# Kernel optimization log

Measured on AMD Instinct MI355X. Metric: run time of the kernel, lower is better.

The kernel has to match this reference:

```python
import jax, jax.numpy as jnp
import numpy as np

B, S, D = 1, 2048, 2048
H, KV, HD = 32, 8, 64
POWER = 100000.0


def _rotary(x):
    # x: [B, h, S, HD]; faithful to RotaryEncoder: freqs = pos / div_term
    rot_dim = HD // 2
    pos = jnp.arange(S, dtype=x.dtype)
    div = POWER ** (jnp.arange(0, HD, 2, dtype=x.dtype) / HD)  # [HD//2]
    freqs = pos[:, None] / div  # [S, HD//2]
    cos, sin = jnp.cos(freqs), jnp.sin(freqs)
    x_rot, x_pass = x[..., :rot_dim], x[..., rot_dim:]
    h = rot_dim // 2
    rot_half = jnp.concatenate([-x_rot[..., h:], x_rot[..., :h]], axis=-1)
    return jnp.concatenate([x_rot * cos + rot_half * sin, x_pass], axis=-1)


def setup_inputs() -> dict:
    key = jax.random.key(0)
    k1, k2, k3 = jax.random.split(key, 3)
    hidden_states = jax.random.normal(k1, (B, S, D), dtype=jnp.float32)
    op_size = H * HD + 2 * KV * HD
    Wqkv = jax.random.normal(k2, (D, op_size), dtype=jnp.float32) * 0.02
    Wo = jax.random.normal(k3, (H * HD, D), dtype=jnp.float32) * 0.02
    causal = jnp.tril(jnp.ones((S, S), dtype=bool))
    attention_mask = jnp.where(causal, 0.0, -1e9).astype(jnp.float32)[None, None]
    return {"hidden_states": hidden_states, "attention_mask": attention_mask,
            "Wqkv": Wqkv, "Wo": Wo}


def reference(hidden_states, attention_mask, Wqkv, Wo):
    groups = H // KV
    qkv = hidden_states @ Wqkv  # [B, S, op_size]
    qpos = H * HD
    q = qkv[..., :qpos].reshape(B, S, H, HD).transpose(0, 2, 1, 3)
    k = qkv[..., qpos:qpos + KV * HD].reshape(B, S, KV, HD).transpose(0, 2, 1, 3)
    v = qkv[..., qpos + KV * HD:].reshape(B, S, KV, HD).transpose(0, 2, 1, 3)
    q = _rotary(q)
    k = _rotary(k)
    k = jnp.repeat(k, groups, axis=1)  # GQA repeat_interleave -> [B, H, S, HD]
    v = jnp.repeat(v, groups, axis=1)
    scores = jnp.einsum('bhqd,bhkd->bhqk', q, k) / jnp.sqrt(jnp.float32(HD))
    scores = scores + attention_mask[..., :S]
    attn = jax.nn.softmax(scores.astype(jnp.float32), axis=-1).astype(v.dtype)
    out = jnp.einsum('bhqk,bhkd->bhqd', attn, v)
    out = out.transpose(0, 2, 1, 3).reshape(B, S, H * HD)
    return out @ Wo
```

## Files before the change

kernel.cpp:

```cpp
#include <hip/hip_runtime.h>
#include <hip/hip_bf16.h>
#include <cstdint>
#include <cstddef>

#define S_LEN 2048
#define D_MODEL 2048
#define NH 32
#define NKV 8
#define HDIM 64
#define OPSZ 3072
#define KOFF 2048
#define VOFF 2560

typedef float    floatx4 __attribute__((ext_vector_type(4)));
typedef __bf16   bf16x8  __attribute__((ext_vector_type(8)));
typedef __bf16   bf16x4  __attribute__((ext_vector_type(4)));
typedef __bf16   bf16_t;
typedef _Float16 f16_t;
typedef _Float16 f16x2   __attribute__((ext_vector_type(2)));
typedef _Float16 f16x4   __attribute__((ext_vector_type(4)));
typedef _Float16 f16x8   __attribute__((ext_vector_type(8)));
typedef __fp16   hfx2    __attribute__((ext_vector_type(2)));

__device__ __forceinline__ void gld16(const void* g, void* l) {
  __builtin_amdgcn_global_load_lds((__attribute__((address_space(1))) void*)(void*)g,
                                   (__attribute__((address_space(3))) void*)l,
                                   16, 0, 0);
}

#define ACQ(N) do { asm volatile("s_waitcnt vmcnt(" #N ")" ::: "memory");        \
                    __builtin_amdgcn_s_barrier();                                \
                    __builtin_amdgcn_sched_barrier(0); } while (0)
#define REL()  do { __builtin_amdgcn_sched_barrier(0);                           \
                    __builtin_amdgcn_s_barrier();                                \
                    __builtin_amdgcn_sched_barrier(0); } while (0)

__global__ __launch_bounds__(256)
void prep_kernel(const float* __restrict__ X, const float* __restrict__ Wqkv,
                 const float* __restrict__ Wo, bf16_t* __restrict__ Xb,
                 bf16_t* __restrict__ WqkvT, bf16_t* __restrict__ WoT) {
  const int bx = blockIdx.x;
  const int k0 = blockIdx.y * 32;
  const int tx = threadIdx.x & 31, ty = threadIdx.x >> 5;
  if (bx < 160) {
    __shared__ float tile[32][33];
    const float* W; bf16_t* Wt; int N, n0;
    if (bx < 96) { W = Wqkv; Wt = WqkvT; N = OPSZ;    n0 = bx * 32; }
    else         { W = Wo;   Wt = WoT;   N = D_MODEL; n0 = (bx - 96) * 32; }
#pragma unroll
    for (int i = 0; i < 32; i += 8)
      tile[ty + i][tx] = W[(size_t)(k0 + ty + i) * N + n0 + tx];
    __syncthreads();
#pragma unroll
    for (int i = 0; i < 32; i += 8)
      Wt[(size_t)(n0 + ty + i) * D_MODEL + k0 + tx] = (bf16_t)tile[tx][ty + i];
  } else {
    const int n0 = (bx - 160) * 32;
#pragma unroll
    for (int i = 0; i < 32; i += 8) {
      const size_t idx = (size_t)(k0 + ty + i) * D_MODEL + n0 + tx;
      Xb[idx] = (bf16_t)X[idx];
    }
  }
}

#define GEMM128_CORE(A_, Bt_, K_, m0_, n0_)                                       \
  const int tid = threadIdx.x;                                                    \
  const int wave = tid >> 6;                                                      \
  const int lane = tid & 63;                                                      \
  const int lane15 = lane & 15;                                                   \
  const int quad = lane >> 4;                                                     \
  const int wm = (wave & 1) * 64;                                                 \
  const int wn = (wave >> 1) * 64;                                                \
  floatx4 acc[4][4];                                                              \
  _Pragma("unroll") for (int i = 0; i < 4; i++)                                   \
    _Pragma("unroll") for (int j = 0; j < 4; j++)                                 \
      acc[i][j] = floatx4{0.f, 0.f, 0.f, 0.f};                                    \
  {                                                                               \
    int srow[4], scol[4];                                                         \
    _Pragma("unroll") for (int i = 0; i < 4; i++) {                               \
      const int c = tid + i * 256;                                                \
      srow[i] = c >> 3;                                                           \
      scol[i] = (((c & 7) * 16) ^ ((srow[i] & 7) << 4)) >> 1;                     \
    }                                                                             \
    const bf16_t* Ab = (A_) + (size_t)(m0_) * (K_);                               \
    const bf16_t* Bb = (Bt_) + (size_t)(n0_) * (K_);                              \
    const int rsw = (lane15 & 7) << 4;                                            \
    auto stage = [&](bf16_t* dA, bf16_t* dB, int k0) {                            \
      _Pragma("unroll") for (int i = 0; i < 4; i++)                               \
        gld16(Ab + (size_t)srow[i] * (K_) + k0 + scol[i],                         \
              dA + (i * 256 + wave * 64) * 8);                                    \
      _Pragma("unroll") for (int i = 0; i < 4; i++)                               \
        gld16(Bb + (size_t)srow[i] * (K_) + k0 + scol[i],                         \
              dB + (i * 256 + wave * 64) * 8);                                    \
    };                                                                            \
    auto comp = [&](const bf16_t* sA, const bf16_t* sB) {                         \
      _Pragma("unroll") for (int kt = 0; kt < 2; kt++) {                          \
        const int off = ((kt * 64 + quad * 16) ^ rsw) >> 1;                       \
        bf16x8 af[4], bfr[4];                                                     \
        _Pragma("unroll") for (int mi = 0; mi < 4; mi++)                          \
          af[mi] = *(const bf16x8*)&sA[(wm + mi * 16 + lane15) * 64 + off];       \
        _Pragma("unroll") for (int ni = 0; ni < 4; ni++)                          \
          bfr[ni] = *(const bf16x8*)&sB[(wn + ni * 16 + lane15) * 64 + off];      \
        _Pragma("unroll") for (int mi = 0; mi < 4; mi++)                          \
          _Pragma("unroll") for (int ni = 0; ni < 4; ni++)                        \
            acc[mi][ni] = __builtin_amdgcn_mfma_f32_16x16x32_bf16(af[mi], bfr[ni],\
                                                                  acc[mi][ni], 0, 0, 0); \
      }                                                                           \
    };                                                                            \
    const int NT = (K_) / 64;                                                     \
    stage(As0, Bs0, 0);                                                           \
    stage(As1, Bs1, 64);                                                          \
    for (int t = 0; t < NT - 2; t += 2) {                                         \
      ACQ(8);                                                                     \
      comp(As0, Bs0);                                                             \
      REL();                                                                      \
      stage(As0, Bs0, (t + 2) * 64);                                              \
      ACQ(8);                                                                     \
      comp(As1, Bs1);                                                             \
      REL();                                                                      \
      stage(As1, Bs1, (t + 3) * 64);                                              \
    }                                                                             \
    ACQ(8);                                                                       \
    comp(As0, Bs0);                                                               \
    ACQ(0);                                                                       \
    comp(As1, Bs1);                                                               \
  }

#define GEMM128_LDS                                                               \
  __shared__ bf16_t As0[128 * 64];                                                \
  __shared__ bf16_t As1[128 * 64];                                                \
  __shared__ bf16_t Bs0[128 * 64];                                                \
  __shared__ bf16_t Bs1[128 * 64];

#define XCD_SWZ(m0_, n0_)                                                         \
  const int gx_ = gridDim.x;                                                      \
  const int id_ = blockIdx.y * gx_ + blockIdx.x;                                  \
  const int cpx_ = (gx_ * gridDim.y) >> 3;                                        \
  const int sid_ = (id_ & 7) * cpx_ + (id_ >> 3);                                 \
  const int m0_ = (sid_ / gx_) * 128;                                             \
  const int n0_ = (sid_ % gx_) * 128;

#define QSCALE 0.18033688011112042f
__global__ __launch_bounds__(256, 2)
void gemm_qkv_rope(const bf16_t* __restrict__ A, const bf16_t* __restrict__ Bt,
                   bf16_t* __restrict__ Qr, bf16_t* __restrict__ Kr,
                   f16_t* __restrict__ VtG) {
  GEMM128_LDS
  XCD_SWZ(m0, n0)
  GEMM128_CORE(A, Bt, D_MODEL, m0, n0)

  const int colbase = n0 + wn;
  const int s0 = m0 + wm;

  if (colbase < VOFF) {
    const bool isQ = (colbase < KOFF);
    const float k2 = 0.51905126483f;
    const float pj0 = exp2f(-(float)lane15 * k2);
    const float pj1 = pj0 * 0.0031622776601684f;
    bf16_t* dst = isQ ? (Qr + ((size_t)(colbase >> 6) * S_LEN) * HDIM)
                      : (Kr + ((size_t)((colbase - KOFF) >> 6) * S_LEN) * HDIM);
    const float qs = isQ ? QSCALE : 1.0f;
#pragma unroll
    for (int mi = 0; mi < 4; mi++) {
#pragma unroll
      for (int r = 0; r < 4; r++) {
        const int s = s0 + mi * 16 + quad * 4 + r;
        const float sf = (float)s;
        float s0s, s0c, s1s, s1c;
        __sincosf(sf * pj0, &s0s, &s0c);
        __sincosf(sf * pj1, &s1s, &s1c);
        const float x0 = acc[mi][0][r], x1 = acc[mi][1][r];
        bf16_t* row = dst + (size_t)s * HDIM + lane15;
        row[0]  = (bf16_t)((x0 * s0c - x1 * s0s) * qs);
        row[16] = (bf16_t)((x1 * s1c + x0 * s1s) * qs);
        row[32] = (bf16_t)(acc[mi][2][r] * qs);
        row[48] = (bf16_t)(acc[mi][3][r] * qs);
      }
    }
  } else {
    const int kvv = (colbase - VOFF) >> 6;
    f16_t* dst = VtG + (size_t)kvv * HDIM * S_LEN;
#pragma unroll
    for (int mi = 0; mi < 4; mi++) {
      const int s = s0 + mi * 16 + quad * 4;
#pragma unroll
      for (int ni = 0; ni < 4; ni++) {
        const int d = ni * 16 + lane15;
        f16x4 tv;
#pragma unroll
        for (int r = 0; r < 4; r++) tv[r] = (f16_t)acc[mi][ni][r];
        *(f16x4*)&dst[(size_t)d * S_LEN + s] = tv;
      }
    }
  }
}

__global__ __launch_bounds__(256, 2)
void gemm_bt_f32out(const bf16_t* __restrict__ A, const bf16_t* __restrict__ Bt,
                    float* __restrict__ C, int M, int N, int K) {
  GEMM128_LDS
  XCD_SWZ(m0, n0)
  GEMM128_CORE(A, Bt, K, m0, n0)

#pragma unroll
  for (int mi = 0; mi < 4; mi++)
#pragma unroll
    for (int r = 0; r < 4; r++) {
      const int row = m0 + wm + mi * 16 + quad * 4 + r;
#pragma unroll
      for (int ni = 0; ni < 4; ni++) {
        const int col = n0 + wn + ni * 16 + lane15;
        C[(size_t)row * N + col] = acc[mi][ni][r];
      }
    }
}

__global__ __launch_bounds__(256, 4)
void flash_kernel(const bf16_t* __restrict__ Qr, const bf16_t* __restrict__ Kr,
                  const f16_t* __restrict__ VtG, bf16_t* __restrict__ attn) {
  __shared__ bf16_t Ks[128 * 64];
  __shared__ f16_t  Vt[64 * 128];

  const int tid = threadIdx.x;
  const int wave = tid >> 6;
  const int lane = tid & 63;
  const int lane15 = lane & 15;
  const int quad = lane >> 4;
  const int bx = blockIdx.x;
  const int h = bx & 31;
  const int qblk = 31 - (bx >> 5);
  const int q0 = qblk * 64;
  const int rq = q0 + wave * 16;
  const int kv = h >> 2;
  const size_t kbase = (size_t)kv * S_LEN * HDIM;
  const size_t vbase = (size_t)kv * HDIM * S_LEN;

  const int krow0 = tid >> 3;
  const int kcol  = ((((tid & 7) * 16) ^ ((krow0 & 7) << 4)) >> 1);
  const int vd0   = tid >> 4;
  const int vcol  = ((((tid & 15) * 16) ^ ((vd0 & 15) << 4)) >> 1);

  const int kswz = (lane15 & 7) << 4;
  const int vswz = lane15 << 4;

  bf16x8 aq[2];
#pragma unroll
  for (int kt = 0; kt < 2; kt++)
    aq[kt] = *(const bf16x8*)&Qr[((size_t)h * S_LEN + rq + lane15) * HDIM + kt * 32 + quad * 8];

  const f16x4 vone = {(f16_t)1.0f, (f16_t)1.0f, (f16_t)1.0f, (f16_t)1.0f};

  floatx4 lacc = floatx4{0.f, 0.f, 0.f, 0.f};
  floatx4 o[4];
#pragma unroll
  for (int dt = 0; dt < 4; dt++) o[dt] = floatx4{0.f, 0.f, 0.f, 0.f};

  const int nk = (qblk + 2) >> 1;

  for (int t = 0; t < nk; ++t) {
    const int p0 = t * 128;
    __syncthreads();
#pragma unroll
    for (int i = 0; i < 4; i++)
      gld16(Kr + kbase + (size_t)(p0 + krow0 + i * 32) * HDIM + kcol,
            &Ks[(i * 256 + wave * 64) * 8]);
#pragma unroll
    for (int i = 0; i < 4; i++)
      gld16(VtG + vbase + (size_t)(vd0 + i * 16) * S_LEN + p0 + vcol,
            &Vt[(i * 256 + wave * 64) * 8]);
    __syncthreads();

    floatx4 sc[8];
#pragma unroll
    for (int nt = 0; nt < 8; nt++) sc[nt] = floatx4{0.f, 0.f, 0.f, 0.f};
#pragma unroll
    for (int kt = 0; kt < 2; kt++) {
#pragma unroll
      for (int nt = 0; nt < 8; nt++) {
        const bf16x8 ak = *(const bf16x8*)&Ks[(nt * 16 + lane15) * 64 +
                                              (((kt * 64 + quad * 16) ^ kswz) >> 1)];
        sc[nt] = __builtin_amdgcn_mfma_f32_16x16x32_bf16(ak, aq[kt], sc[nt], 0, 0, 0);
      }
    }

    if (p0 + 127 > rq) {
#pragma unroll
      for (int nt = 0; nt < 8; nt++)
#pragma unroll
        for (int r = 0; r < 4; r++) {
          const int kpos = p0 + nt * 16 + quad * 4 + r;
          const int qrow = rq + lane15;
          if (kpos > qrow) sc[nt][r] = -1e30f;
        }
    }

    f16x4 ph[8];
#pragma unroll
    for (int nt = 0; nt < 8; nt++) {
      const float e0 = __builtin_amdgcn_exp2f(sc[nt][0]);
      const float e1 = __builtin_amdgcn_exp2f(sc[nt][1]);
      const float e2 = __builtin_amdgcn_exp2f(sc[nt][2]);
      const float e3 = __builtin_amdgcn_exp2f(sc[nt][3]);
      const hfx2 lo_ = __builtin_amdgcn_cvt_pkrtz(e0, e1);
      const hfx2 hi_ = __builtin_amdgcn_cvt_pkrtz(e2, e3);
      const f16x2 lo = __builtin_bit_cast(f16x2, lo_);
      const f16x2 hi = __builtin_bit_cast(f16x2, hi_);
      ph[nt] = __builtin_shufflevector(lo, hi, 0, 1, 2, 3);
    }

#pragma unroll
    for (int kt4 = 0; kt4 < 8; kt4++) {
      lacc = __builtin_amdgcn_mfma_f32_16x16x16f16(vone, ph[kt4], lacc, 0, 0, 0);
#pragma unroll
      for (int dt = 0; dt < 4; dt++) {
        const f16x4 av = *(const f16x4*)&Vt[(dt * 16 + lane15) * 128 +
                                            (((kt4 * 32 + quad * 8) ^ vswz) >> 1)];
        o[dt] = __builtin_amdgcn_mfma_f32_16x16x16f16(av, ph[kt4], o[dt], 0, 0, 0);
      }
    }
  }

  const float inv = 1.0f / lacc[0];
  const int s = rq + lane15;
#pragma unroll
  for (int dt = 0; dt < 4; dt++) {
    bf16x4 tv;
#pragma unroll
    for (int r = 0; r < 4; r++) tv[r] = (bf16_t)(o[dt][r] * inv);
    *(bf16x4*)&attn[(size_t)s * D_MODEL + h * HDIM + dt * 16 + quad * 4] = tv;
  }
}

extern "C" void kernel_launch(void* const* d_in, const int* in_sizes, int n_in,
                              void* d_out, int out_size, void* d_ws, size_t ws_size,
                              hipStream_t stream) {
  (void)in_sizes; (void)n_in; (void)out_size; (void)ws_size;
  const float* hidden = (const float*)d_in[0];
  const float* Wqkv = (const float*)d_in[2];
  const float* Wo   = (const float*)d_in[3];
  float* out = (float*)d_out;

  char* ws = (char*)d_ws;
  size_t off = 0;
  auto alloc = [&](size_t bytes) -> void* {
    void* p = ws + off;
    off += (bytes + 255) & ~(size_t)255;
    return p;
  };
  bf16_t* Xb    = (bf16_t*)alloc((size_t)S_LEN * D_MODEL * 2);
  bf16_t* WqkvT = (bf16_t*)alloc((size_t)OPSZ * D_MODEL * 2);
  bf16_t* WoT   = (bf16_t*)alloc((size_t)D_MODEL * D_MODEL * 2);
  bf16_t* Qr    = (bf16_t*)alloc((size_t)NH * S_LEN * HDIM * 2);
  bf16_t* Kr    = (bf16_t*)alloc((size_t)NKV * S_LEN * HDIM * 2);
  f16_t*  VtG   = (f16_t*) alloc((size_t)NKV * HDIM * S_LEN * 2);
  bf16_t* attn  = (bf16_t*)alloc((size_t)S_LEN * D_MODEL * 2);

  prep_kernel<<<dim3(224, 64), 256, 0, stream>>>(hidden, Wqkv, Wo, Xb, WqkvT, WoT);
  gemm_qkv_rope<<<dim3(OPSZ / 128, S_LEN / 128), 256, 0, stream>>>(Xb, WqkvT, Qr, Kr, VtG);
  flash_kernel<<<dim3(32 * NH), 256, 0, stream>>>(Qr, Kr, VtG, attn);
  gemm_bt_f32out<<<dim3(D_MODEL / 128, S_LEN / 128), 256, 0, stream>>>(attn, WoT, out, S_LEN, D_MODEL, D_MODEL);
}
```

Measured before the change: 203.0 us.

## Store K and V in MFMA-fragment layout and read directly from global

The QKV GEMM epilogue now writes K and V in a pre-swizzled fragment layout that matches the MFMA operand order. The flash kernel can then load its K and V fragments straight from global memory into registers, dropping the LDS staging and both __syncthreads per tile. The cost is that each of the four waves re-reads the same K/V from global or L2 with no LDS sharing. The K/V epilogue also now uses scattered 2-byte stores.

Result: slower. 230.4 us (+13.5%).

```diff
diff --git a/kernel.cpp b/kernel.cpp
--- a/kernel.cpp
+++ b/kernel.cpp
@@ -144,8 +144,8 @@
 #define QSCALE 0.18033688011112042f
 __global__ __launch_bounds__(256, 2)
 void gemm_qkv_rope(const bf16_t* __restrict__ A, const bf16_t* __restrict__ Bt,
-                   bf16_t* __restrict__ Qr, bf16_t* __restrict__ Kr,
-                   f16_t* __restrict__ VtG) {
+                   bf16_t* __restrict__ Qr, bf16_t* __restrict__ KF,
+                   f16_t* __restrict__ VF) {
   GEMM128_LDS
   XCD_SWZ(m0, n0)
   GEMM128_CORE(A, Bt, D_MODEL, m0, n0)
@@ -153,14 +153,11 @@
   const int colbase = n0 + wn;
   const int s0 = m0 + wm;
 
-  if (colbase < VOFF) {
-    const bool isQ = (colbase < KOFF);
+  if (colbase < KOFF) {
     const float k2 = 0.51905126483f;
     const float pj0 = exp2f(-(float)lane15 * k2);
     const float pj1 = pj0 * 0.0031622776601684f;
-    bf16_t* dst = isQ ? (Qr + ((size_t)(colbase >> 6) * S_LEN) * HDIM)
-                      : (Kr + ((size_t)((colbase - KOFF) >> 6) * S_LEN) * HDIM);
-    const float qs = isQ ? QSCALE : 1.0f;
+    bf16_t* dst = Qr + ((size_t)(colbase >> 6) * S_LEN) * HDIM;
 #pragma unroll
     for (int mi = 0; mi < 4; mi++) {
 #pragma unroll
@@ -172,25 +169,51 @@
         __sincosf(sf * pj1, &s1s, &s1c);
         const float x0 = acc[mi][0][r], x1 = acc[mi][1][r];
         bf16_t* row = dst + (size_t)s * HDIM + lane15;
-        row[0]  = (bf16_t)((x0 * s0c - x1 * s0s) * qs);
-        row[16] = (bf16_t)((x1 * s1c + x0 * s1s) * qs);
-        row[32] = (bf16_t)(acc[mi][2][r] * qs);
-        row[48] = (bf16_t)(acc[mi][3][r] * qs);
+        row[0]  = (bf16_t)((x0 * s0c - x1 * s0s) * QSCALE);
+        row[16] = (bf16_t)((x1 * s1c + x0 * s1s) * QSCALE);
+        row[32] = (bf16_t)(acc[mi][2][r] * QSCALE);
+        row[48] = (bf16_t)(acc[mi][3][r] * QSCALE);
+      }
+    }
+  } else if (colbase < VOFF) {
+    const float k2 = 0.51905126483f;
+    const float pj0 = exp2f(-(float)lane15 * k2);
+    const float pj1 = pj0 * 0.0031622776601684f;
+    bf16_t* dst = KF + (size_t)((colbase - KOFF) >> 6) * (S_LEN * HDIM);
+    const int jj = lane15 & 7;
+    const int sb = lane15 >> 3;
+#pragma unroll
+    for (int mi = 0; mi < 4; mi++) {
+#pragma unroll
+      for (int r = 0; r < 4; r++) {
+        const int s = s0 + mi * 16 + quad * 4 + r;
+        const float sf = (float)s;
+        float s0s, s0c, s1s, s1c;
+        __sincosf(sf * pj0, &s0s, &s0c);
+        __sincosf(sf * pj1, &s1s, &s1c);
+        const float x0 = acc[mi][0][r], x1 = acc[mi][1][r];
+        const int t7 = s >> 7, ntq = (s >> 4) & 7;
+        const int l0 = quad * 4 + r;
+        bf16_t* pk0 = dst + ((t7 * 2 + 0) * 8 + ntq) * 512;
+        bf16_t* pk1 = dst + ((t7 * 2 + 1) * 8 + ntq) * 512;
+        pk0[(l0 + 16 * sb) * 8 + jj]       = (bf16_t)(x0 * s0c - x1 * s0s);
+        pk0[(l0 + 16 * (2 + sb)) * 8 + jj] = (bf16_t)(x1 * s1c + x0 * s1s);
+        pk1[(l0 + 16 * sb) * 8 + jj]       = (bf16_t)acc[mi][2][r];
+        pk1[(l0 + 16 * (2 + sb)) * 8 + jj] = (bf16_t)acc[mi][3][r];
       }
     }
   } else {
     const int kvv = (colbase - VOFF) >> 6;
-    f16_t* dst = VtG + (size_t)kvv * HDIM * S_LEN;
+    f16_t* dst = VF + (size_t)kvv * (S_LEN * HDIM);
 #pragma unroll
     for (int mi = 0; mi < 4; mi++) {
-      const int s = s0 + mi * 16 + quad * 4;
+      const int s16 = (s0 + mi * 16) >> 4;
 #pragma unroll
       for (int ni = 0; ni < 4; ni++) {
-        const int d = ni * 16 + lane15;
         f16x4 tv;
 #pragma unroll
         for (int r = 0; r < 4; r++) tv[r] = (f16_t)acc[mi][ni][r];
-        *(f16x4*)&dst[(size_t)d * S_LEN + s] = tv;
+        *(f16x4*)&dst[(((size_t)s16 * 4 + ni) * 64 + lane) * 4] = tv;
       }
     }
   }
@@ -217,11 +240,8 @@
 }
 
 __global__ __launch_bounds__(256, 4)
-void flash_kernel(const bf16_t* __restrict__ Qr, const bf16_t* __restrict__ Kr,
-                  const f16_t* __restrict__ VtG, bf16_t* __restrict__ attn) {
-  __shared__ bf16_t Ks[128 * 64];
-  __shared__ f16_t  Vt[64 * 128];
-
+void flash_kernel(const bf16_t* __restrict__ Qr, const bf16_t* __restrict__ KF,
+                  const f16_t* __restrict__ VF, bf16_t* __restrict__ attn) {
   const int tid = threadIdx.x;
   const int wave = tid >> 6;
   const int lane = tid & 63;
@@ -233,16 +253,9 @@
   const int q0 = qblk * 64;
   const int rq = q0 + wave * 16;
   const int kv = h >> 2;
-  const size_t kbase = (size_t)kv * S_LEN * HDIM;
-  const size_t vbase = (size_t)kv * HDIM * S_LEN;
-
-  const int krow0 = tid >> 3;
-  const int kcol  = ((((tid & 7) * 16) ^ ((krow0 & 7) << 4)) >> 1);
-  const int vd0   = tid >> 4;
-  const int vcol  = ((((tid & 15) * 16) ^ ((vd0 & 15) << 4)) >> 1);
-
-  const int kswz = (lane15 & 7) << 4;
-  const int vswz = lane15 << 4;
+
+  const bf16_t* kf = KF + (size_t)kv * (S_LEN * HDIM) + lane * 8;
+  const f16_t*  vf = VF + (size_t)kv * (S_LEN * HDIM) + lane * 4;
 
   bf16x8 aq[2];
 #pragma unroll
@@ -260,16 +273,6 @@
 
   for (int t = 0; t < nk; ++t) {
     const int p0 = t * 128;
-    __syncthreads();
-#pragma unroll
-    for (int i = 0; i < 4; i++)
-      gld16(Kr + kbase + (size_t)(p0 + krow0 + i * 32) * HDIM + kcol,
-            &Ks[(i * 256 + wave * 64) * 8]);
-#pragma unroll
-    for (int i = 0; i < 4; i++)
-      gld16(VtG + vbase + (size_t)(vd0 + i * 16) * S_LEN + p0 + vcol,
-            &Vt[(i * 256 + wave * 64) * 8]);
-    __syncthreads();
 
     floatx4 sc[8];
 #pragma unroll
@@ -278,8 +281,7 @@
     for (int kt = 0; kt < 2; kt++) {
 #pragma unroll
       for (int nt = 0; nt < 8; nt++) {
-        const bf16x8 ak = *(const bf16x8*)&Ks[(nt * 16 + lane15) * 64 +
-                                              (((kt * 64 + quad * 16) ^ kswz) >> 1)];
+        const bf16x8 ak = *(const bf16x8*)(kf + (size_t)(((t * 2 + kt) * 8 + nt)) * 512);
         sc[nt] = __builtin_amdgcn_mfma_f32_16x16x32_bf16(ak, aq[kt], sc[nt], 0, 0, 0);
       }
     }
@@ -314,8 +316,7 @@
       lacc = __builtin_amdgcn_mfma_f32_16x16x16f16(vone, ph[kt4], lacc, 0, 0, 0);
 #pragma unroll
       for (int dt = 0; dt < 4; dt++) {
-        const f16x4 av = *(const f16x4*)&Vt[(dt * 16 + lane15) * 128 +
-                                            (((kt4 * 32 + quad * 8) ^ vswz) >> 1)];
+        const f16x4 av = *(const f16x4*)(vf + (size_t)(((t * 8 + kt4) * 4 + dt)) * 256);
         o[dt] = __builtin_amdgcn_mfma_f32_16x16x16f16(av, ph[kt4], o[dt], 0, 0, 0);
       }
     }
@@ -352,12 +353,12 @@
   bf16_t* WqkvT = (bf16_t*)alloc((size_t)OPSZ * D_MODEL * 2);
   bf16_t* WoT   = (bf16_t*)alloc((size_t)D_MODEL * D_MODEL * 2);
   bf16_t* Qr    = (bf16_t*)alloc((size_t)NH * S_LEN * HDIM * 2);
-  bf16_t* Kr    = (bf16_t*)alloc((size_t)NKV * S_LEN * HDIM * 2);
-  f16_t*  VtG   = (f16_t*) alloc((size_t)NKV * HDIM * S_LEN * 2);
+  bf16_t* KF    = (bf16_t*)alloc((size_t)NKV * S_LEN * HDIM * 2);
+  f16_t*  VF    = (f16_t*) alloc((size_t)NKV * HDIM * S_LEN * 2);
   bf16_t* attn  = (bf16_t*)alloc((size_t)S_LEN * D_MODEL * 2);
 
   prep_kernel<<<dim3(224, 64), 256, 0, stream>>>(hidden, Wqkv, Wo, Xb, WqkvT, WoT);
-  gemm_qkv_rope<<<dim3(OPSZ / 128, S_LEN / 128), 256, 0, stream>>>(Xb, WqkvT, Qr, Kr, VtG);
-  flash_kernel<<<dim3(32 * NH), 256, 0, stream>>>(Qr, Kr, VtG, attn);
+  gemm_qkv_rope<<<dim3(OPSZ / 128, S_LEN / 128), 256, 0, stream>>>(Xb, WqkvT, Qr, KF, VF);
+  flash_kernel<<<dim3(32 * NH), 256, 0, stream>>>(Qr, KF, VF, attn);
   gemm_bt_f32out<<<dim3(D_MODEL / 128, S_LEN / 128), 256, 0, stream>>>(attn, WoT, out, S_LEN, D_MODEL, D_MODEL);
 }
```

## Restructure flash attention to 128-row query tiles with 32x32 MFMA

Applied to the files above, without the earlier changes.

Each attention block now handles 128 query rows, 32 per wave, instead of 64, which halves the grid. QK^T and PV switch from 16x16 to 32x32 MFMA instructions. The row sum is accumulated in scalar adds plus a cross-half shuffle rather than an extra ones-MFMA. This doubles reuse of each staged K/V tile and cuts LDS traffic per FLOP, at the cost of more registers (launch bounds lowered to 2), fewer blocks, and coarser causal load balance, which the new block ordering tries to offset.

After: 201.8 us, median of 2. About the same (-0.6%).

```diff
diff --git a/kernel.cpp b/kernel.cpp
--- a/kernel.cpp
+++ b/kernel.cpp
@@ -12,7 +12,8 @@
 #define KOFF 2048
 #define VOFF 2560
 
-typedef float    floatx4 __attribute__((ext_vector_type(4)));
+typedef float    floatx4  __attribute__((ext_vector_type(4)));
+typedef float    floatx16 __attribute__((ext_vector_type(16)));
 typedef __bf16   bf16x8  __attribute__((ext_vector_type(8)));
 typedef __bf16   bf16x4  __attribute__((ext_vector_type(4)));
 typedef __bf16   bf16_t;
@@ -216,7 +217,7 @@
     }
 }
 
-__global__ __launch_bounds__(256, 4)
+__global__ __launch_bounds__(256, 2)
 void flash_kernel(const bf16_t* __restrict__ Qr, const bf16_t* __restrict__ Kr,
                   const f16_t* __restrict__ VtG, bf16_t* __restrict__ attn) {
   __shared__ bf16_t Ks[128 * 64];
@@ -225,38 +226,37 @@
   const int tid = threadIdx.x;
   const int wave = tid >> 6;
   const int lane = tid & 63;
-  const int lane15 = lane & 15;
-  const int quad = lane >> 4;
+  const int l31 = lane & 31;
+  const int half = lane >> 5;
   const int bx = blockIdx.x;
   const int h = bx & 31;
-  const int qblk = 31 - (bx >> 5);
-  const int q0 = qblk * 64;
-  const int rq = q0 + wave * 16;
+  const int bq = bx >> 5;
+  const int qblk = (bq < 8) ? (15 - bq) : (bq - 8);
+  const int q0 = qblk * 128;
+  const int rq = q0 + wave * 32;
   const int kv = h >> 2;
   const size_t kbase = (size_t)kv * S_LEN * HDIM;
   const size_t vbase = (size_t)kv * HDIM * S_LEN;
 
   const int krow0 = tid >> 3;
-  const int kcol  = ((((tid & 7) * 16) ^ ((krow0 & 7) << 4)) >> 1);
+  const int kcol  = ((((tid & 7) * 16) ^ (((tid >> 3) & 7) << 4)) >> 1);
   const int vd0   = tid >> 4;
   const int vcol  = ((((tid & 15) * 16) ^ ((vd0 & 15) << 4)) >> 1);
 
-  const int kswz = (lane15 & 7) << 4;
-  const int vswz = lane15 << 4;
-
-  bf16x8 aq[2];
-#pragma unroll
-  for (int kt = 0; kt < 2; kt++)
-    aq[kt] = *(const bf16x8*)&Qr[((size_t)h * S_LEN + rq + lane15) * HDIM + kt * 32 + quad * 8];
-
-  const f16x4 vone = {(f16_t)1.0f, (f16_t)1.0f, (f16_t)1.0f, (f16_t)1.0f};
-
-  floatx4 lacc = floatx4{0.f, 0.f, 0.f, 0.f};
-  floatx4 o[4];
-#pragma unroll
-  for (int dt = 0; dt < 4; dt++) o[dt] = floatx4{0.f, 0.f, 0.f, 0.f};
-
-  const int nk = (qblk + 2) >> 1;
+  const int kswz = (l31 & 7) << 4;
+  const int vswz = (l31 & 15) << 4;
+
+  bf16x8 aq[4];
+#pragma unroll
+  for (int kt = 0; kt < 4; kt++)
+    aq[kt] = *(const bf16x8*)&Qr[((size_t)h * S_LEN + rq + l31) * HDIM + kt * 16 + half * 8];
+
+  floatx16 o0, o1;
+#pragma unroll
+  for (int i = 0; i < 16; i++) { o0[i] = 0.f; o1[i] = 0.f; }
+  floatx4 ls = floatx4{0.f, 0.f, 0.f, 0.f};
+
+  const int nk = qblk + 1;
 
   for (int t = 0; t < nk; ++t) {
     const int p0 = t * 128;
@@ -271,64 +271,68 @@
             &Vt[(i * 256 + wave * 64) * 8]);
     __syncthreads();
 
-    floatx4 sc[8];
-#pragma unroll
-    for (int nt = 0; nt < 8; nt++) sc[nt] = floatx4{0.f, 0.f, 0.f, 0.f};
-#pragma unroll
-    for (int kt = 0; kt < 2; kt++) {
-#pragma unroll
-      for (int nt = 0; nt < 8; nt++) {
-        const bf16x8 ak = *(const bf16x8*)&Ks[(nt * 16 + lane15) * 64 +
-                                              (((kt * 64 + quad * 16) ^ kswz) >> 1)];
-        sc[nt] = __builtin_amdgcn_mfma_f32_16x16x32_bf16(ak, aq[kt], sc[nt], 0, 0, 0);
-      }
-    }
-
-    if (p0 + 127 > rq) {
-#pragma unroll
-      for (int nt = 0; nt < 8; nt++)
-#pragma unroll
-        for (int r = 0; r < 4; r++) {
-          const int kpos = p0 + nt * 16 + quad * 4 + r;
-          const int qrow = rq + lane15;
-          if (kpos > qrow) sc[nt][r] = -1e30f;
+#pragma unroll
+    for (int nt = 0; nt < 4; nt++) {
+      floatx16 sc;
+#pragma unroll
+      for (int i = 0; i < 16; i++) sc[i] = 0.f;
+#pragma unroll
+      for (int kt = 0; kt < 4; kt++) {
+        const bf16x8 ak = *(const bf16x8*)&Ks[(nt * 32 + l31) * 64 +
+                                              (((kt * 32 + half * 16) ^ kswz) >> 1)];
+        sc = __builtin_amdgcn_mfma_f32_32x32x16_bf16(ak, aq[kt], sc, 0, 0, 0);
+      }
+
+      if (p0 + nt * 32 + 31 > rq) {
+        const int qrow = rq + l31;
+        const int kb = p0 + nt * 32 + 4 * half;
+#pragma unroll
+        for (int r = 0; r < 16; r++) {
+          const int kpos = kb + (r & 3) + 8 * (r >> 2);
+          if (kpos > qrow) sc[r] = -1e30f;
         }
-    }
-
-    f16x4 ph[8];
-#pragma unroll
-    for (int nt = 0; nt < 8; nt++) {
-      const float e0 = __builtin_amdgcn_exp2f(sc[nt][0]);
-      const float e1 = __builtin_amdgcn_exp2f(sc[nt][1]);
-      const float e2 = __builtin_amdgcn_exp2f(sc[nt][2]);
-      const float e3 = __builtin_amdgcn_exp2f(sc[nt][3]);
-      const hfx2 lo_ = __builtin_amdgcn_cvt_pkrtz(e0, e1);
-      const hfx2 hi_ = __builtin_amdgcn_cvt_pkrtz(e2, e3);
-      const f16x2 lo = __builtin_bit_cast(f16x2, lo_);
-      const f16x2 hi = __builtin_bit_cast(f16x2, hi_);
-      ph[nt] = __builtin_shufflevector(lo, hi, 0, 1, 2, 3);
-    }
-
-#pragma unroll
-    for (int kt4 = 0; kt4 < 8; kt4++) {
-      lacc = __builtin_amdgcn_mfma_f32_16x16x16f16(vone, ph[kt4], lacc, 0, 0, 0);
-#pragma unroll
-      for (int dt = 0; dt < 4; dt++) {
-        const f16x4 av = *(const f16x4*)&Vt[(dt * 16 + lane15) * 128 +
-                                            (((kt4 * 32 + quad * 8) ^ vswz) >> 1)];
-        o[dt] = __builtin_amdgcn_mfma_f32_16x16x16f16(av, ph[kt4], o[dt], 0, 0, 0);
-      }
-    }
-  }
-
-  const float inv = 1.0f / lacc[0];
-  const int s = rq + lane15;
-#pragma unroll
-  for (int dt = 0; dt < 4; dt++) {
-    bf16x4 tv;
-#pragma unroll
-    for (int r = 0; r < 4; r++) tv[r] = (bf16_t)(o[dt][r] * inv);
-    *(bf16x4*)&attn[(size_t)s * D_MODEL + h * HDIM + dt * 16 + quad * 4] = tv;
+      }
+
+      f16x4 ph[4];
+#pragma unroll
+      for (int g = 0; g < 4; g++) {
+        const float e0 = __builtin_amdgcn_exp2f(sc[4 * g + 0]);
+        const float e1 = __builtin_amdgcn_exp2f(sc[4 * g + 1]);
+        const float e2 = __builtin_amdgcn_exp2f(sc[4 * g + 2]);
+        const float e3 = __builtin_amdgcn_exp2f(sc[4 * g + 3]);
+        ls[g] += (e0 + e1) + (e2 + e3);
+        const hfx2 lo_ = __builtin_amdgcn_cvt_pkrtz(e0, e1);
+        const hfx2 hi_ = __builtin_amdgcn_cvt_pkrtz(e2, e3);
+        ph[g] = __builtin_shufflevector(__builtin_bit_cast(f16x2, lo_),
+                                        __builtin_bit_cast(f16x2, hi_), 0, 1, 2, 3);
+      }
+
+#pragma unroll
+      for (int g = 0; g < 4; g++) {
+        const int cb = nt * 64 + g * 16 + half * 8;
+        const f16x4 av0 = *(const f16x4*)&Vt[(l31) * 128 + ((cb ^ vswz) >> 1)];
+        const f16x4 av1 = *(const f16x4*)&Vt[(32 + l31) * 128 + ((cb ^ vswz) >> 1)];
+        o0 = __builtin_amdgcn_mfma_f32_32x32x8f16(av0, ph[g], o0, 0, 0, 0);
+        o1 = __builtin_amdgcn_mfma_f32_32x32x8f16(av1, ph[g], o1, 0, 0, 0);
+      }
+    }
+  }
+
+  float lsum = ls[0] + ls[1] + ls[2] + ls[3];
+  lsum += __shfl_xor(lsum, 32);
+  const float inv = 1.0f / lsum;
+  const int s = rq + l31;
+#pragma unroll
+  for (int rg = 0; rg < 4; rg++) {
+    bf16x4 t0, t1;
+#pragma unroll
+    for (int j = 0; j < 4; j++) {
+      t0[j] = (bf16_t)(o0[rg * 4 + j] * inv);
+      t1[j] = (bf16_t)(o1[rg * 4 + j] * inv);
+    }
+    const int d = rg * 8 + half * 4;
+    *(bf16x4*)&attn[(size_t)s * D_MODEL + h * HDIM + d] = t0;
+    *(bf16x4*)&attn[(size_t)s * D_MODEL + h * HDIM + 32 + d] = t1;
   }
 }
 
@@ -358,6 +362,6 @@
 
   prep_kernel<<<dim3(224, 64), 256, 0, stream>>>(hidden, Wqkv, Wo, Xb, WqkvT, WoT);
   gemm_qkv_rope<<<dim3(OPSZ / 128, S_LEN / 128), 256, 0, stream>>>(Xb, WqkvT, Qr, Kr, VtG);
-  flash_kernel<<<dim3(32 * NH), 256, 0, stream>>>(Qr, Kr, VtG, attn);
+  flash_kernel<<<dim3(16 * NH), 256, 0, stream>>>(Qr, Kr, VtG, attn);
   gemm_bt_f32out<<<dim3(D_MODEL / 128, S_LEN / 128), 256, 0, stream>>>(attn, WoT, out, S_LEN, D_MODEL, D_MODEL);
 }
```
